# Performance work log

Measured on AMD Instinct MI355X. Metric: run time of the kernel, lower is better.

Reference implementation:

```python
import jax, jax.numpy as jnp
import numpy as np

N_NODES = 100000
N_EDGES = 1600000
IN_FEATS = 128
OUT_FEATS = 256
K = 32


def setup_inputs() -> dict:
    key = jax.random.key(0)
    ks = jax.random.split(key, 8)
    feat = jax.random.normal(ks[0], (N_NODES, IN_FEATS), dtype=jnp.float32)
    # MaxK sparsified activations: nonnegative values (post-ReLU top-k)
    topk_values = jax.random.uniform(ks[1], (N_NODES, K), dtype=jnp.float32)
    topk_indices = jax.random.randint(ks[2], (N_NODES, K), 0, IN_FEATS, dtype=jnp.int32)
    # CSR expanded to COO: sorted row ids emulate indptr ordering
    row = jnp.sort(jax.random.randint(ks[3], (N_EDGES,), 0, N_NODES, dtype=jnp.int32))
    col = jax.random.randint(ks[4], (N_EDGES,), 0, N_NODES, dtype=jnp.int32)
    # in-degrees clamped to min 1.0, as in set_graph_data
    deg = jax.ops.segment_sum(jnp.ones((N_EDGES,), jnp.float32), row, num_segments=N_NODES)
    degrees = jnp.maximum(deg, 1.0)
    gain = float(np.sqrt(2.0))  # calculate_gain('relu')
    bnd_n = gain * np.sqrt(6.0 / (IN_FEATS + OUT_FEATS))
    W_neigh = jax.random.uniform(ks[5], (IN_FEATS, OUT_FEATS), jnp.float32, -bnd_n, bnd_n)
    W_self = jax.random.uniform(ks[6], (IN_FEATS, OUT_FEATS), jnp.float32, -bnd_n, bnd_n)
    bnd_b = 1.0 / np.sqrt(IN_FEATS)
    b_self = jax.random.uniform(ks[7], (OUT_FEATS,), jnp.float32, -bnd_b, bnd_b)
    return {"feat": feat, "topk_values": topk_values, "topk_indices": topk_indices,
            "row": row, "col": col, "degrees": degrees,
            "W_neigh": W_neigh, "W_self": W_self, "b_self": b_self}


def reference(feat, topk_values, topk_indices, row, col, degrees, W_neigh, W_self, b_self):
    n = feat.shape[0]
    # Scatter top-k sparse features back to dense [N, in_feats]
    # (real top-k indices are unique per row, so add == set; add is deterministic)
    rows = jnp.arange(n, dtype=jnp.int32)[:, None]
    x_sparse = jnp.zeros((n, IN_FEATS), feat.dtype).at[rows, topk_indices].add(topk_values)
    # CSR SpMM with all-ones edge values + degree normalization (mean aggregation)
    gathered = x_sparse[col]                                  # [E, in_feats]
    agg = jax.ops.segment_sum(gathered, row, num_segments=n)  # [N, in_feats]
    agg = agg / degrees[:, None]
    # lin_before_mp is False (in_feats <= out_feats): linear after aggregation
    h_neigh = agg @ W_neigh                                    # [N, out_feats]
    rst = feat @ W_self + b_self + h_neigh
    return rst
```

## Files before the change

kernel.cpp:

```cpp
#include <hip/hip_runtime.h>
#include <stdint.h>

#define IN_FEATS 128
#define OUT_FEATS 256
#define TOPK 32
#define BM 128
#define BN 128
#define BK 64
#define KTOT 256

typedef float f32x4 __attribute__((ext_vector_type(4)));
typedef short bf16x8 __attribute__((ext_vector_type(8)));

__device__ __forceinline__ unsigned short f2bf(float x) {
    unsigned u = __float_as_uint(x);
    u += 0x7FFFu + ((u >> 16) & 1u);
    return (unsigned short)(u >> 16);
}

__device__ __forceinline__ void gload16(const void* g, void* l) {
    __builtin_amdgcn_global_load_lds(
        (const __attribute__((address_space(1))) unsigned*)g,
        (__attribute__((address_space(3))) unsigned*)l, 16, 0, 0);
}

__global__ void k_scatter(const float* __restrict__ vals, const int* __restrict__ idxs,
                          unsigned short* __restrict__ xsp, int n_nodes) {
    __shared__ float lds[2 * IN_FEATS];
    int t = threadIdx.x;
    int n0 = blockIdx.x * 2;
    lds[t] = 0.f;
    __syncthreads();
    if (t < 2 * TOPK) {
        int h = t >> 5;
        int k = t & 31;
        int n = n0 + h;
        if (n < n_nodes) {
            float v = vals[(size_t)n * TOPK + k];
            int ix = idxs[(size_t)n * TOPK + k];
            atomicAdd(&lds[h * IN_FEATS + ix], v);
        }
    }
    __syncthreads();
    int h2 = t >> 7;
    int f = t & 127;
    int n = n0 + h2;
    if (n < n_nodes) xsp[(size_t)n * IN_FEATS + f] = f2bf(lds[t]);
}

__global__ void k_weights(const float* __restrict__ Wn, const float* __restrict__ Ws,
                          unsigned short* __restrict__ WT) {
    int idx = blockIdx.x * 256 + threadIdx.x;
    int n = idx >> 8;
    int k = idx & 255;
    float v = (k < IN_FEATS) ? Wn[(size_t)k * OUT_FEATS + n]
                             : Ws[(size_t)(k - IN_FEATS) * OUT_FEATS + n];
    WT[idx] = f2bf(v);
}

__global__ void k_indptr(const int* __restrict__ row, int* __restrict__ indptr,
                         int n_nodes, int n_edges) {
    int e = blockIdx.x * 256 + threadIdx.x;
    if (e >= n_edges) return;
    int r = row[e];
    int rp = (e == 0) ? -1 : row[e - 1];
    for (int x = rp + 1; x <= r; ++x) indptr[x] = e;
    if (e == n_edges - 1)
        for (int x = r + 1; x <= n_nodes; ++x) indptr[x] = n_edges;
}

__global__ __launch_bounds__(256) void k_aggregate(
    const unsigned short* __restrict__ xsp,
    const float* __restrict__ feat,
    const int* __restrict__ indptr, const int* __restrict__ col,
    unsigned short* __restrict__ Acat, int n_nodes) {
    int t = threadIdx.x;
    int node = blockIdx.x * 4 + (t >> 6);
    if (node >= n_nodes) return;
    int lane = t & 63;
    int eg = lane >> 4, fi = lane & 15;
    int e0 = indptr[node], e1 = indptr[node + 1];

    float acc[8] = {0.f, 0.f, 0.f, 0.f, 0.f, 0.f, 0.f, 0.f};
    int elast = (e1 > e0) ? (e1 - 1) : e0;
    for (int base = e0; base < e1; base += 8) {
        int ea = base + eg;
        int eb = base + 4 + eg;
        float sa = (ea < e1) ? 1.f : 0.f;
        float sb = (eb < e1) ? 1.f : 0.f;
        int ca = col[ea < elast ? ea : elast];
        int cb = col[eb < elast ? eb : elast];
        uint4 ua = *(const uint4*)(xsp + (size_t)ca * IN_FEATS + fi * 8);
        uint4 ub = *(const uint4*)(xsp + (size_t)cb * IN_FEATS + fi * 8);
        unsigned pa[4] = {ua.x, ua.y, ua.z, ua.w};
        unsigned pb[4] = {ub.x, ub.y, ub.z, ub.w};
#pragma unroll
        for (int i = 0; i < 4; ++i) {
            acc[2 * i]     = fmaf(sa, __uint_as_float(pa[i] << 16), acc[2 * i]);
            acc[2 * i + 1] = fmaf(sa, __uint_as_float(pa[i] & 0xFFFF0000u), acc[2 * i + 1]);
            acc[2 * i]     = fmaf(sb, __uint_as_float(pb[i] << 16), acc[2 * i]);
            acc[2 * i + 1] = fmaf(sb, __uint_as_float(pb[i] & 0xFFFF0000u), acc[2 * i + 1]);
        }
    }
#pragma unroll
    for (int i = 0; i < 8; ++i) {
        acc[i] += __shfl_down(acc[i], 16, 64);
        acc[i] += __shfl_down(acc[i], 32, 64);
    }
    if (eg == 0) {
        int cnt = e1 - e0;
        float inv = 1.0f / (float)(cnt > 0 ? cnt : 1);
        unsigned o[4];
#pragma unroll
        for (int i = 0; i < 4; ++i) {
            unsigned lo = f2bf(acc[2 * i] * inv);
            unsigned hi = f2bf(acc[2 * i + 1] * inv);
            o[i] = lo | (hi << 16);
        }
        *(uint4*)(Acat + (size_t)node * KTOT + fi * 8) = *(uint4*)&o[0];
    }
    float2 fv = *(const float2*)(feat + (size_t)node * IN_FEATS + lane * 2);
    unsigned pk = (unsigned)f2bf(fv.x) | ((unsigned)f2bf(fv.y) << 16);
    *(unsigned*)(Acat + (size_t)node * KTOT + IN_FEATS + lane * 2) = pk;
}

__global__ __launch_bounds__(256) void k_gemm(
    const unsigned short* __restrict__ Acat,
    const unsigned short* __restrict__ WT,
    const float* __restrict__ bias,
    float* __restrict__ out, int n_nodes) {
    __shared__ __align__(16) unsigned short Ash[BM * BK];
    __shared__ __align__(16) unsigned short Bsh[BN * BK];
    int t = threadIdx.x;
    int m0 = blockIdx.x * BM;
    int n0 = blockIdx.y * BN;
    int lane = t & 63;
    int w = t >> 6;
    int wr = w >> 1, wc = w & 1;
    int lrow = lane & 15, quad = lane >> 4;

    f32x4 acc[4][4];
#pragma unroll
    for (int i = 0; i < 4; ++i)
#pragma unroll
        for (int j = 0; j < 4; ++j)
            acc[i][j] = (f32x4){0.f, 0.f, 0.f, 0.f};

    for (int kk = 0; kk < KTOT; kk += BK) {
#pragma unroll
        for (int p = 0; p < 4; ++p) {
            int c = p * 256 + t;
            int row = c >> 3;
            int q = (c & 7) ^ (row & 7);
            int nodeA = m0 + row;
            if (nodeA >= n_nodes) nodeA = n_nodes - 1;
            gload16(Acat + (size_t)nodeA * KTOT + kk + q * 8, &Ash[(size_t)c * 8]);
            gload16(WT + (size_t)(n0 + row) * KTOT + kk + q * 8, &Bsh[(size_t)c * 8]);
        }
        __syncthreads();

#pragma unroll
        for (int ks = 0; ks < 2; ++ks) {
            bf16x8 af[4], bfr[4];
#pragma unroll
            for (int mi = 0; mi < 4; ++mi) {
                int r = wr * 64 + mi * 16 + lrow;
                int q = (ks * 4 + quad) ^ (r & 7);
                af[mi] = *(const bf16x8*)&Ash[(r * 8 + q) * 8];
            }
#pragma unroll
            for (int ni = 0; ni < 4; ++ni) {
                int r = wc * 64 + ni * 16 + lrow;
                int q = (ks * 4 + quad) ^ (r & 7);
                bfr[ni] = *(const bf16x8*)&Bsh[(r * 8 + q) * 8];
            }
#pragma unroll
            for (int mi = 0; mi < 4; ++mi)
#pragma unroll
                for (int ni = 0; ni < 4; ++ni)
                    acc[mi][ni] = __builtin_amdgcn_mfma_f32_16x16x32_bf16(
                        af[mi], bfr[ni], acc[mi][ni], 0, 0, 0);
        }
        __syncthreads();
    }

#pragma unroll
    for (int mi = 0; mi < 4; ++mi) {
        int gm = m0 + wr * 64 + mi * 16 + quad * 4;
#pragma unroll
        for (int ni = 0; ni < 4; ++ni) {
            int go = n0 + wc * 64 + ni * 16 + lrow;
            float b = bias[go];
#pragma unroll
            for (int r = 0; r < 4; ++r) {
                int node = gm + r;
                if (node < n_nodes)
                    out[(size_t)node * OUT_FEATS + go] = acc[mi][ni][r] + b;
            }
        }
    }
}

extern "C" void kernel_launch(void* const* d_in, const int* in_sizes, int n_in,
                              void* d_out, int out_size, void* d_ws, size_t ws_size,
                              hipStream_t stream) {
    const float* feat = (const float*)d_in[0];
    const float* tkv  = (const float*)d_in[1];
    const int*   tki  = (const int*)d_in[2];
    const int*   row  = (const int*)d_in[3];
    const int*   col  = (const int*)d_in[4];
    const float* Wn   = (const float*)d_in[6];
    const float* Ws   = (const float*)d_in[7];
    const float* bias = (const float*)d_in[8];
    float* out = (float*)d_out;

    int n_nodes = in_sizes[5];
    int n_edges = in_sizes[3];

    unsigned short* xsp  = (unsigned short*)d_ws;
    unsigned short* Acat = xsp + (size_t)n_nodes * IN_FEATS;
    unsigned short* WT   = Acat + (size_t)n_nodes * KTOT;
    int* indptr = (int*)(WT + (size_t)OUT_FEATS * KTOT);

    k_scatter<<<(n_nodes + 1) / 2, 256, 0, stream>>>(tkv, tki, xsp, n_nodes);
    k_weights<<<256, 256, 0, stream>>>(Wn, Ws, WT);
    k_indptr<<<(n_edges + 255) / 256, 256, 0, stream>>>(row, indptr, n_nodes, n_edges);
    k_aggregate<<<(n_nodes + 3) / 4, 256, 0, stream>>>(xsp, feat, indptr, col, Acat, n_nodes);
    dim3 g3((n_nodes + BM - 1) / BM, OUT_FEATS / BN);
    k_gemm<<<g3, 256, 0, stream>>>(Acat, WT, bias, out, n_nodes);
}
```

Before: 313.5 us.

## Aggregate from packed top-k pairs with LDS atomics instead of dense rows

Replaces the dense bf16 scatter of top-k activations with a packed 32-entry (bf16 value, 7-bit index) array per node. The aggregation kernel gathers these compact entries per neighbor and scatter-adds them into a per-node LDS accumulator with shared-memory atomics, halving gathered bytes per edge (128B vs 256B). The trade is LDS atomic contention and an extra block-wide barrier in place of register accumulation and shuffle reduction.

```diff
diff --git a/kernel.cpp b/kernel.cpp
--- a/kernel.cpp
+++ b/kernel.cpp
@@ -24,28 +24,11 @@
         (__attribute__((address_space(3))) unsigned*)l, 16, 0, 0);
 }
 
-__global__ void k_scatter(const float* __restrict__ vals, const int* __restrict__ idxs,
-                          unsigned short* __restrict__ xsp, int n_nodes) {
-    __shared__ float lds[2 * IN_FEATS];
-    int t = threadIdx.x;
-    int n0 = blockIdx.x * 2;
-    lds[t] = 0.f;
-    __syncthreads();
-    if (t < 2 * TOPK) {
-        int h = t >> 5;
-        int k = t & 31;
-        int n = n0 + h;
-        if (n < n_nodes) {
-            float v = vals[(size_t)n * TOPK + k];
-            int ix = idxs[(size_t)n * TOPK + k];
-            atomicAdd(&lds[h * IN_FEATS + ix], v);
-        }
-    }
-    __syncthreads();
-    int h2 = t >> 7;
-    int f = t & 127;
-    int n = n0 + h2;
-    if (n < n_nodes) xsp[(size_t)n * IN_FEATS + f] = f2bf(lds[t]);
+__global__ void k_pack(const float* __restrict__ vals, const int* __restrict__ idxs,
+                       unsigned* __restrict__ packed, int total) {
+    int i = blockIdx.x * 256 + threadIdx.x;
+    if (i >= total) return;
+    packed[i] = ((unsigned)f2bf(vals[i]) << 16) | ((unsigned)idxs[i] & 127u);
 }
 
 __global__ void k_weights(const float* __restrict__ Wn, const float* __restrict__ Ws,
@@ -70,18 +53,28 @@
 }
 
 __global__ __launch_bounds__(256) void k_aggregate(
-    const unsigned short* __restrict__ xsp,
+    const unsigned* __restrict__ packed,
     const float* __restrict__ feat,
     const int* __restrict__ indptr, const int* __restrict__ col,
     unsigned short* __restrict__ Acat, int n_nodes) {
+    __shared__ float acc[4 * IN_FEATS];
     int t = threadIdx.x;
-    int node = blockIdx.x * 4 + (t >> 6);
-    if (node >= n_nodes) return;
+    int wv = t >> 6;
     int lane = t & 63;
+    int node = blockIdx.x * 4 + wv;
+    bool valid = node < n_nodes;
+    int nodec = valid ? node : (n_nodes - 1);
+
+    acc[t] = 0.f;
+    acc[t + 256] = 0.f;
+    __syncthreads();
+
+    int e0 = indptr[nodec];
+    int e1 = indptr[nodec + 1];
+    if (!valid) e1 = e0;
     int eg = lane >> 4, fi = lane & 15;
-    int e0 = indptr[node], e1 = indptr[node + 1];
-
-    float acc[8] = {0.f, 0.f, 0.f, 0.f, 0.f, 0.f, 0.f, 0.f};
+    float* macc = acc + wv * IN_FEATS;
+
     int elast = (e1 > e0) ? (e1 - 1) : e0;
     for (int base = e0; base < e1; base += 8) {
         int ea = base + eg;
@@ -90,38 +83,32 @@
         float sb = (eb < e1) ? 1.f : 0.f;
         int ca = col[ea < elast ? ea : elast];
         int cb = col[eb < elast ? eb : elast];
-        uint4 ua = *(const uint4*)(xsp + (size_t)ca * IN_FEATS + fi * 8);
-        uint4 ub = *(const uint4*)(xsp + (size_t)cb * IN_FEATS + fi * 8);
-        unsigned pa[4] = {ua.x, ua.y, ua.z, ua.w};
-        unsigned pb[4] = {ub.x, ub.y, ub.z, ub.w};
-#pragma unroll
-        for (int i = 0; i < 4; ++i) {
-            acc[2 * i]     = fmaf(sa, __uint_as_float(pa[i] << 16), acc[2 * i]);
-            acc[2 * i + 1] = fmaf(sa, __uint_as_float(pa[i] & 0xFFFF0000u), acc[2 * i + 1]);
-            acc[2 * i]     = fmaf(sb, __uint_as_float(pb[i] << 16), acc[2 * i]);
-            acc[2 * i + 1] = fmaf(sb, __uint_as_float(pb[i] & 0xFFFF0000u), acc[2 * i + 1]);
-        }
-    }
-#pragma unroll
-    for (int i = 0; i < 8; ++i) {
-        acc[i] += __shfl_down(acc[i], 16, 64);
-        acc[i] += __shfl_down(acc[i], 32, 64);
-    }
-    if (eg == 0) {
-        int cnt = e1 - e0;
-        float inv = 1.0f / (float)(cnt > 0 ? cnt : 1);
-        unsigned o[4];
-#pragma unroll
-        for (int i = 0; i < 4; ++i) {
-            unsigned lo = f2bf(acc[2 * i] * inv);
-            unsigned hi = f2bf(acc[2 * i + 1] * inv);
-            o[i] = lo | (hi << 16);
-        }
-        *(uint4*)(Acat + (size_t)node * KTOT + fi * 8) = *(uint4*)&o[0];
-    }
-    float2 fv = *(const float2*)(feat + (size_t)node * IN_FEATS + lane * 2);
-    unsigned pk = (unsigned)f2bf(fv.x) | ((unsigned)f2bf(fv.y) << 16);
-    *(unsigned*)(Acat + (size_t)node * KTOT + IN_FEATS + lane * 2) = pk;
+        uint2 ua = *(const uint2*)(packed + (size_t)ca * TOPK + fi * 2);
+        uint2 ub = *(const uint2*)(packed + (size_t)cb * TOPK + fi * 2);
+        atomicAdd(&macc[ua.x & 127u], __uint_as_float(ua.x & 0xFFFF0000u) * sa);
+        atomicAdd(&macc[ua.y & 127u], __uint_as_float(ua.y & 0xFFFF0000u) * sa);
+        atomicAdd(&macc[ub.x & 127u], __uint_as_float(ub.x & 0xFFFF0000u) * sb);
+        atomicAdd(&macc[ub.y & 127u], __uint_as_float(ub.y & 0xFFFF0000u) * sb);
+    }
+    __syncthreads();
+
+    if (valid) {
+        if (eg == 0) {
+            int cnt = e1 - e0;
+            float inv = 1.0f / (float)(cnt > 0 ? cnt : 1);
+            unsigned o[4];
+#pragma unroll
+            for (int i = 0; i < 4; ++i) {
+                unsigned lo = f2bf(macc[fi * 8 + 2 * i] * inv);
+                unsigned hi = f2bf(macc[fi * 8 + 2 * i + 1] * inv);
+                o[i] = lo | (hi << 16);
+            }
+            *(uint4*)(Acat + (size_t)node * KTOT + fi * 8) = *(uint4*)&o[0];
+        }
+        float2 fv = *(const float2*)(feat + (size_t)node * IN_FEATS + lane * 2);
+        unsigned pk = (unsigned)f2bf(fv.x) | ((unsigned)f2bf(fv.y) << 16);
+        *(unsigned*)(Acat + (size_t)node * KTOT + IN_FEATS + lane * 2) = pk;
+    }
 }
 
 __global__ __launch_bounds__(256) void k_gemm(
@@ -217,15 +204,16 @@
     int n_nodes = in_sizes[5];
     int n_edges = in_sizes[3];
 
-    unsigned short* xsp  = (unsigned short*)d_ws;
-    unsigned short* Acat = xsp + (size_t)n_nodes * IN_FEATS;
+    unsigned* packed = (unsigned*)d_ws;
+    unsigned short* Acat = (unsigned short*)(packed + (size_t)n_nodes * TOPK);
     unsigned short* WT   = Acat + (size_t)n_nodes * KTOT;
     int* indptr = (int*)(WT + (size_t)OUT_FEATS * KTOT);
 
-    k_scatter<<<(n_nodes + 1) / 2, 256, 0, stream>>>(tkv, tki, xsp, n_nodes);
+    int total = n_nodes * TOPK;
+    k_pack<<<(total + 255) / 256, 256, 0, stream>>>(tkv, tki, packed, total);
     k_weights<<<256, 256, 0, stream>>>(Wn, Ws, WT);
     k_indptr<<<(n_edges + 255) / 256, 256, 0, stream>>>(row, indptr, n_nodes, n_edges);
-    k_aggregate<<<(n_nodes + 3) / 4, 256, 0, stream>>>(xsp, feat, indptr, col, Acat, n_nodes);
+    k_aggregate<<<(n_nodes + 3) / 4, 256, 0, stream>>>(packed, feat, indptr, col, Acat, n_nodes);
     dim3 g3((n_nodes + BM - 1) / BM, OUT_FEATS / BN);
     k_gemm<<<g3, 256, 0, stream>>>(Acat, WT, bias, out, n_nodes);
 }
```

New measurement: 524.7 us. 67.4% more time.
